# Performance work log

Measured on AMD Instinct MI355X. Metric: run time of the kernel, lower is better.

Reference implementation:

```python
import jax, jax.numpy as jnp
import numpy as np

N_NODES = 100000
N_EDGES = 1600000
HIDDEN = 64


def gcn_conv(x, edge_index, W, b):
    """PyG GCNConv: add self-loops, symmetric deg^{-1/2} normalization, scatter-add."""
    n = x.shape[0]
    h = x @ W  # [N, F_out]
    loop = jnp.arange(n, dtype=edge_index.dtype)
    src = jnp.concatenate([edge_index[0], loop])  # [E+N]
    dst = jnp.concatenate([edge_index[1], loop])
    deg = jax.ops.segment_sum(jnp.ones_like(dst, dtype=h.dtype), dst, num_segments=n)
    dinv = jnp.where(deg > 0, jax.lax.rsqrt(jnp.maximum(deg, 1e-12)), 0.0)
    norm = dinv[src] * dinv[dst]  # [E+N]
    msg = h[src] * norm[:, None]  # gather + scale
    out = jax.ops.segment_sum(msg, dst, num_segments=n)  # scatter-add
    return out + b


def setup_inputs() -> dict:
    key = jax.random.key(0)
    k = jax.random.split(key, 6)
    x = jax.random.normal(k[0], (N_NODES, HIDDEN), dtype=jnp.float32)
    edge_index = jax.random.randint(k[1], (2, N_EDGES), 0, N_NODES, dtype=jnp.int32)
    s = 1.0 / np.sqrt(HIDDEN)
    W1 = jax.random.normal(k[2], (HIDDEN, HIDDEN), dtype=jnp.float32) * s
    b1 = jnp.zeros((HIDDEN,), dtype=jnp.float32)
    W2 = jax.random.normal(k[3], (HIDDEN, HIDDEN), dtype=jnp.float32) * s
    b2 = jnp.zeros((HIDDEN,), dtype=jnp.float32)
    return {"x": x, "edge_index": edge_index, "W1": W1, "b1": b1, "W2": W2, "b2": b2}


def reference(x, edge_index, W1, b1, W2, b2):
    # Faithful to source: conv1 applied twice, relu, dropout (eval -> identity), conv2, log_softmax.
    h = gcn_conv(x, edge_index, W1, b1)
    h = jax.nn.relu(gcn_conv(h, edge_index, W1, b1))
    # F.dropout(training=self.training): identity in eval mode
    h = gcn_conv(h, edge_index, W2, b2)
    return jax.nn.log_softmax(h, axis=1)
```

## Files before the change

kernel.cpp:

```cpp
#include <hip/hip_runtime.h>
#include <hip/hip_bf16.h>

#define HID 64

typedef float f32x4 __attribute__((ext_vector_type(4)));

__device__ __forceinline__ unsigned short f2bf(float f) {
    unsigned u = __float_as_uint(f);
    return (unsigned short)((u + 0x7fffu + ((u >> 16) & 1u)) >> 16);
}
__device__ __forceinline__ void acc8(float* a, uint4 v) {
    a[0] += __uint_as_float(v.x << 16);
    a[1] += __uint_as_float(v.x & 0xffff0000u);
    a[2] += __uint_as_float(v.y << 16);
    a[3] += __uint_as_float(v.y & 0xffff0000u);
    a[4] += __uint_as_float(v.z << 16);
    a[5] += __uint_as_float(v.z & 0xffff0000u);
    a[6] += __uint_as_float(v.w << 16);
    a[7] += __uint_as_float(v.w & 0xffff0000u);
}


__global__ __launch_bounds__(256) void hist_part_kernel(
    const int* __restrict__ dst, int* __restrict__ cnt, int E, int psz) {
    int part = blockIdx.x & 7, chunk = blockIdx.x >> 3;
    int i = chunk * 256 + threadIdx.x;
    if (i >= E) return;
    int d = __builtin_nontemporal_load(&dst[i]);
    if (d / psz == part) atomicAdd(&cnt[d], 1);
}

__global__ __launch_bounds__(256) void bsum_kernel(const int* __restrict__ cnt,
                                                   int* __restrict__ bsums, int N) {
    __shared__ int s[256];
    int tid = threadIdx.x, i = blockIdx.x * 256 + tid;
    s[tid] = (i < N) ? cnt[i] : 0;
    __syncthreads();
    for (int o = 128; o > 0; o >>= 1) {
        if (tid < o) s[tid] += s[tid + o];
        __syncthreads();
    }
    if (tid == 0) bsums[blockIdx.x] = s[0];
}

__global__ __launch_bounds__(512) void scan_bsums_kernel(int* __restrict__ bsums, int nblk) {
    __shared__ int s[512];
    int tid = threadIdx.x;
    int orig = (tid < nblk) ? bsums[tid] : 0;
    s[tid] = orig;
    __syncthreads();
    for (int off = 1; off < 512; off <<= 1) {
        int v = (tid >= off) ? s[tid - off] : 0;
        __syncthreads();
        s[tid] += v;
        __syncthreads();
    }
    if (tid < nblk) bsums[tid] = s[tid] - orig;
}

__global__ __launch_bounds__(256) void rowptr_kernel(
    const int* __restrict__ cnt, const int* __restrict__ bsums,
    int4* __restrict__ nodeinfo, int* __restrict__ cursor, int N) {
    __shared__ int s[256];
    int tid = threadIdx.x, i = blockIdx.x * 256 + tid;
    int c = (i < N) ? cnt[i] : 0;
    s[tid] = c;
    __syncthreads();
    for (int off = 1; off < 256; off <<= 1) {
        int v = (tid >= off) ? s[tid - off] : 0;
        __syncthreads();
        s[tid] += v;
        __syncthreads();
    }
    if (i < N) {
        int excl = s[tid] - c + bsums[blockIdx.x];
        cursor[i] = excl;
        int4 ni;
        ni.x = excl;
        ni.y = c;
        ni.z = (int)__float_as_uint(rsqrtf((float)c + 1.0f));
        ni.w = 0;
        nodeinfo[i] = ni;
    }
}

__global__ __launch_bounds__(256) void fill_part_kernel(
    const int* __restrict__ src, const int* __restrict__ dst,
    int* __restrict__ cursor, int* __restrict__ col, int E, int psz) {
    int part = blockIdx.x & 7, chunk = blockIdx.x >> 3;
    int i = chunk * 256 + threadIdx.x;
    if (i >= E) return;
    int d = __builtin_nontemporal_load(&dst[i]);
    if (d / psz == part) {
        int s = __builtin_nontemporal_load(&src[i]);
        int p = atomicAdd(&cursor[d], 1);
        __builtin_nontemporal_store(s, &col[p]);
    }
}

__device__ __forceinline__ void gather64(
    const uint4* __restrict__ g4, const int* __restrict__ col,
    int beg, int deg, int n, int N, int lane, float* t) {
    int eighth = lane >> 3, fo = lane & 7;
    float a0[8] = {}, a1[8] = {};
    for (int base = 0; base < deg; base += 64) {
        int rem = deg - base; rem = rem > 64 ? 64 : rem;
        int c = (lane < rem) ? __builtin_nontemporal_load(&col[beg + base + lane]) : N;
        int groups = (rem + 7) >> 3;
        int j = 0;
        for (; j + 2 <= groups; j += 2) {
            int s0 = __shfl(c, 8 * (j + 0) + eighth, 64);
            int s1 = __shfl(c, 8 * (j + 1) + eighth, 64);
            uint4 v0 = g4[(size_t)s0 * 8 + fo];
            uint4 v1 = g4[(size_t)s1 * 8 + fo];
            acc8(a0, v0); acc8(a1, v1);
        }
        if (j < groups) {
            int s0 = __shfl(c, 8 * j + eighth, 64);
            uint4 v0 = g4[(size_t)s0 * 8 + fo];
            acc8(a0, v0);
        }
    }
    float sf[8] = {};
    acc8(sf, g4[(size_t)n * 8 + fo]);
#pragma unroll
    for (int k = 0; k < 8; ++k) {
        float s = a0[k] + a1[k];
        s += __shfl_xor(s, 8, 64);
        s += __shfl_xor(s, 16, 64);
        s += __shfl_xor(s, 32, 64);
        t[k] = s + sf[k];
    }
}


__global__ __launch_bounds__(256) void gemm_scale_kernel(
    const float* __restrict__ X, const float* __restrict__ W,
    const int4* __restrict__ nodeinfo, unsigned short* __restrict__ g, int N) {
    int tid = threadIdx.x, w = tid >> 6, lane = tid & 63;
    float Wreg[64];
#pragma unroll
    for (int k = 0; k < HID; ++k) Wreg[k] = W[k * HID + lane];
    int ngrp = (N + 4) / 4;
    for (int grp = blockIdx.x; grp < ngrp; grp += gridDim.x) {
        int row = grp * 4 + w;
        if (row > N) continue;
        if (row == N) { __builtin_nontemporal_store((unsigned short)0, &g[(size_t)N * HID + lane]); continue; }
        float xv = __builtin_nontemporal_load(&X[(size_t)row * HID + lane]);
        float dn = __uint_as_float(__builtin_amdgcn_readfirstlane((unsigned)nodeinfo[row].z));
        float acc = 0.f;
#pragma unroll
        for (int k = 0; k < HID; ++k) acc = fmaf(__shfl(xv, k, 64), Wreg[k], acc);
        __builtin_nontemporal_store(f2bf(acc * dn), &g[(size_t)row * HID + lane]);
    }
}


template <bool RELU>
__global__ __launch_bounds__(256) void agg_gemm_kernel(
    const unsigned short* __restrict__ g_in, const int4* __restrict__ nodeinfo,
    const int* __restrict__ col, const float* __restrict__ bias,
    const float* __restrict__ W, unsigned short* __restrict__ g_out, int N) {
    int tid = threadIdx.x, w = tid >> 6, lane = tid & 63;
    int fo = lane & 7;
    float Wreg[64];
#pragma unroll
    for (int k = 0; k < HID; ++k) Wreg[k] = W[k * HID + lane];
    float bb[8];
#pragma unroll
    for (int j = 0; j < 8; ++j) bb[j] = bias[8 * fo + j];
    const uint4* g4 = (const uint4*)g_in;
    int ngrp = (N + 4) / 4;
    for (int grp = blockIdx.x; grp < ngrp; grp += gridDim.x) {
        int n = grp * 4 + w;
        if (n > N) continue;
        if (n == N) { __builtin_nontemporal_store((unsigned short)0, &g_out[(size_t)N * HID + lane]); continue; }
        int4 ni = nodeinfo[n];
        int beg  = __builtin_amdgcn_readfirstlane(ni.x);
        int deg  = __builtin_amdgcn_readfirstlane(ni.y);
        float dn = __uint_as_float(__builtin_amdgcn_readfirstlane((unsigned)ni.z));
        float t[8];
        gather64(g4, col, beg, deg, n, N, lane, t);
        float o[8];
#pragma unroll
        for (int j = 0; j < 8; ++j) {
            o[j] = fmaf(dn, t[j], bb[j]);
            if (RELU) o[j] = fmaxf(o[j], 0.f);
        }
        float acc = 0.f;
#pragma unroll
        for (int q = 0; q < 8; ++q)
#pragma unroll
            for (int j = 0; j < 8; ++j)
                acc = fmaf(__shfl(o[j], q, 64), Wreg[8 * q + j], acc);
        __builtin_nontemporal_store(f2bf(acc * dn), &g_out[(size_t)n * HID + lane]);
    }
}


__global__ __launch_bounds__(256) void agg_lsm_kernel(
    const unsigned short* __restrict__ g_in, const int4* __restrict__ nodeinfo,
    const int* __restrict__ col, const float* __restrict__ bias,
    float* __restrict__ out, int N) {
    int tid = threadIdx.x;
    int n = blockIdx.x * 4 + (tid >> 6);
    if (n >= N) return;
    int lane = tid & 63;
    int eighth = lane >> 3, fo = lane & 7;
    int4 ni = nodeinfo[n];
    int beg  = __builtin_amdgcn_readfirstlane(ni.x);
    int deg  = __builtin_amdgcn_readfirstlane(ni.y);
    float dn = __uint_as_float(__builtin_amdgcn_readfirstlane((unsigned)ni.z));
    const uint4* g4 = (const uint4*)g_in;
    float t[8];
    gather64(g4, col, beg, deg, n, N, lane, t);
    float v[8];
#pragma unroll
    for (int k = 0; k < 8; ++k) v[k] = fmaf(dn, t[k], bias[8 * fo + k]);
    float mx = v[0];
#pragma unroll
    for (int k = 1; k < 8; ++k) mx = fmaxf(mx, v[k]);
    mx = fmaxf(mx, __shfl_xor(mx, 1, 64));
    mx = fmaxf(mx, __shfl_xor(mx, 2, 64));
    mx = fmaxf(mx, __shfl_xor(mx, 4, 64));
    float sum = 0.f;
#pragma unroll
    for (int k = 0; k < 8; ++k) sum += expf(v[k] - mx);
    sum += __shfl_xor(sum, 1, 64);
    sum += __shfl_xor(sum, 2, 64);
    sum += __shfl_xor(sum, 4, 64);
    float ls = mx + logf(sum);
    if (eighth == 0) {
        f32x4 o0 = {v[0] - ls, v[1] - ls, v[2] - ls, v[3] - ls};
        f32x4 o1 = {v[4] - ls, v[5] - ls, v[6] - ls, v[7] - ls};
        f32x4* op = (f32x4*)out;
        __builtin_nontemporal_store(o0, &op[(size_t)n * 16 + 2 * fo]);
        __builtin_nontemporal_store(o1, &op[(size_t)n * 16 + 2 * fo + 1]);
    }
}


static inline size_t alignup(size_t x) { return (x + 255) & ~(size_t)255; }

extern "C" void kernel_launch(void* const* d_in, const int* in_sizes, int n_in,
                              void* d_out, int out_size, void* d_ws, size_t ws_size,
                              hipStream_t stream) {
    const float* x  = (const float*)d_in[0];
    const int*   ei = (const int*)d_in[1];
    const float* W1 = (const float*)d_in[2];
    const float* b1 = (const float*)d_in[3];
    const float* W2 = (const float*)d_in[4];
    const float* b2 = (const float*)d_in[5];

    const int N = in_sizes[0] / HID;
    const int E = in_sizes[1] / 2;
    const int* src = ei;
    const int* dst = ei + E;

    const int nblk = (N + 255) / 256;
    const int psz  = (N + 7) / 8;

    char* w = (char*)d_ws;
    unsigned short* gA       = (unsigned short*)w; w += alignup((size_t)(N + 1) * HID * 2);
    unsigned short* gB       = (unsigned short*)w; w += alignup((size_t)(N + 1) * HID * 2);
    int4*           nodeinfo = (int4*)w;           w += alignup((size_t)N * 16);
    int*            cnt      = (int*)w;            w += alignup((size_t)N * 4);
    int*            cursor   = (int*)w;            w += alignup((size_t)N * 4);
    int*            col      = (int*)w;            w += alignup((size_t)E * 4);
    int*            bsums    = (int*)w;            w += alignup((size_t)nblk * 4);

    const int egrid  = (E + 255) / 256;
    const int ngrid  = (N + 3) / 4;
    const int gsgrid = 2048;

    (void)hipMemsetAsync(cnt, 0, (size_t)N * sizeof(int), stream);
    hist_part_kernel<<<egrid * 8, 256, 0, stream>>>(dst, cnt, E, psz);
    bsum_kernel<<<nblk, 256, 0, stream>>>(cnt, bsums, N);
    scan_bsums_kernel<<<1, 512, 0, stream>>>(bsums, nblk);
    rowptr_kernel<<<nblk, 256, 0, stream>>>(cnt, bsums, nodeinfo, cursor, N);
    fill_part_kernel<<<egrid * 8, 256, 0, stream>>>(src, dst, cursor, col, E, psz);

    gemm_scale_kernel<<<gsgrid, 256, 0, stream>>>(x, W1, nodeinfo, gA, N);
    agg_gemm_kernel<false><<<gsgrid, 256, 0, stream>>>(gA, nodeinfo, col, b1, W1, gB, N);
    agg_gemm_kernel<true><<<gsgrid, 256, 0, stream>>>(gB, nodeinfo, col, b1, W2, gA, N);
    agg_lsm_kernel<<<ngrid, 256, 0, stream>>>(gA, nodeinfo, col, b2, (float*)d_out, N);
}
```

Before: 498.1 us.

## Pack W as bf16 registers, prefetch first col chunk, persist LSM kernel

The fused aggregate-GEMM kernels now keep W as packed bf16 pairs in 32 registers instead of 64 floats. The 64x64 product is done as a local partial product followed by a butterfly shuffle reduction, and the kernel gets a launch-bounds occupancy hint. The first column-index chunk is loaded before the gather loop so it can overlap setup work. The first GEMM now stages W and the x row in shared memory instead of using register shuffles. The log-softmax kernel becomes a grid-stride persistent kernel, the padding-row zeroing moves to memsets, and the col store becomes a normal store. Rounding W to bf16 adds some precision error.

```diff
diff --git a/kernel.cpp b/kernel.cpp
--- a/kernel.cpp
+++ b/kernel.cpp
@@ -94,18 +94,18 @@
     if (d / psz == part) {
         int s = __builtin_nontemporal_load(&src[i]);
         int p = atomicAdd(&cursor[d], 1);
-        __builtin_nontemporal_store(s, &col[p]);
-    }
-}
-
-__device__ __forceinline__ void gather64(
+        col[p] = s;
+    }
+}
+
+__device__ __forceinline__ void gather64_pre(
     const uint4* __restrict__ g4, const int* __restrict__ col,
-    int beg, int deg, int n, int N, int lane, float* t) {
+    int beg, int deg, int c, int n, int N, int lane, float* t) {
     int eighth = lane >> 3, fo = lane & 7;
     float a0[8] = {}, a1[8] = {};
-    for (int base = 0; base < deg; base += 64) {
-        int rem = deg - base; rem = rem > 64 ? 64 : rem;
-        int c = (lane < rem) ? __builtin_nontemporal_load(&col[beg + base + lane]) : N;
+    int base = 0;
+    while (true) {
+        int rem = deg - base; if (rem > 64) rem = 64;
         int groups = (rem + 7) >> 3;
         int j = 0;
         for (; j + 2 <= groups; j += 2) {
@@ -120,6 +120,10 @@
             uint4 v0 = g4[(size_t)s0 * 8 + fo];
             acc8(a0, v0);
         }
+        base += 64;
+        if (base >= deg) break;
+        int r2 = deg - base;
+        c = (lane < r2) ? __builtin_nontemporal_load(&col[beg + base + lane]) : N;
     }
     float sf[8] = {};
     acc8(sf, g4[(size_t)n * 8 + fo]);
@@ -137,63 +141,96 @@
 __global__ __launch_bounds__(256) void gemm_scale_kernel(
     const float* __restrict__ X, const float* __restrict__ W,
     const int4* __restrict__ nodeinfo, unsigned short* __restrict__ g, int N) {
-    int tid = threadIdx.x, w = tid >> 6, lane = tid & 63;
-    float Wreg[64];
-#pragma unroll
-    for (int k = 0; k < HID; ++k) Wreg[k] = W[k * HID + lane];
-    int ngrp = (N + 4) / 4;
+    __shared__ float Ws[HID * HID];
+    __shared__ float xs[4][HID];
+    int tid = threadIdx.x;
+    for (int i = tid; i < HID * HID; i += 256) Ws[i] = W[i];
+    __syncthreads();
+    int w = tid >> 6, c = tid & 63;
+    float* xsw = xs[w];
+    int ngrp = (N + 3) / 4;
     for (int grp = blockIdx.x; grp < ngrp; grp += gridDim.x) {
         int row = grp * 4 + w;
-        if (row > N) continue;
-        if (row == N) { __builtin_nontemporal_store((unsigned short)0, &g[(size_t)N * HID + lane]); continue; }
-        float xv = __builtin_nontemporal_load(&X[(size_t)row * HID + lane]);
-        float dn = __uint_as_float(__builtin_amdgcn_readfirstlane((unsigned)nodeinfo[row].z));
+        if (row >= N) continue;
+        xsw[c] = __builtin_nontemporal_load(&X[(size_t)row * HID + c]);
+        float dn = __uint_as_float((unsigned)__builtin_amdgcn_readfirstlane(nodeinfo[row].z));
         float acc = 0.f;
 #pragma unroll
-        for (int k = 0; k < HID; ++k) acc = fmaf(__shfl(xv, k, 64), Wreg[k], acc);
-        __builtin_nontemporal_store(f2bf(acc * dn), &g[(size_t)row * HID + lane]);
+        for (int k = 0; k < HID; ++k) acc = fmaf(xsw[k], Ws[k * HID + c], acc);
+        __builtin_nontemporal_store(f2bf(acc * dn), &g[(size_t)row * HID + c]);
     }
 }
 
 
 template <bool RELU>
-__global__ __launch_bounds__(256) void agg_gemm_kernel(
+__global__ __launch_bounds__(256, 4) void agg_gemm_kernel(
     const unsigned short* __restrict__ g_in, const int4* __restrict__ nodeinfo,
     const int* __restrict__ col, const float* __restrict__ bias,
     const float* __restrict__ W, unsigned short* __restrict__ g_out, int N) {
     int tid = threadIdx.x, w = tid >> 6, lane = tid & 63;
-    int fo = lane & 7;
-    float Wreg[64];
-#pragma unroll
-    for (int k = 0; k < HID; ++k) Wreg[k] = W[k * HID + lane];
+    int s = lane & 7, q = lane >> 3;
+    unsigned Wp[32];
+#pragma unroll
+    for (int j = 0; j < 8; ++j)
+#pragma unroll
+        for (int i2 = 0; i2 < 4; ++i2) {
+            float w0 = W[(8 * s + j) * HID + 8 * q + 2 * i2];
+            float w1 = W[(8 * s + j) * HID + 8 * q + 2 * i2 + 1];
+            Wp[j * 4 + i2] = (unsigned)f2bf(w0) | ((unsigned)f2bf(w1) << 16);
+        }
     float bb[8];
 #pragma unroll
-    for (int j = 0; j < 8; ++j) bb[j] = bias[8 * fo + j];
+    for (int j = 0; j < 8; ++j) bb[j] = bias[8 * s + j];
     const uint4* g4 = (const uint4*)g_in;
-    int ngrp = (N + 4) / 4;
+    const int ngrp = (N + 3) / 4;
     for (int grp = blockIdx.x; grp < ngrp; grp += gridDim.x) {
         int n = grp * 4 + w;
-        if (n > N) continue;
-        if (n == N) { __builtin_nontemporal_store((unsigned short)0, &g_out[(size_t)N * HID + lane]); continue; }
+        if (n >= N) continue;
         int4 ni = nodeinfo[n];
-        int beg  = __builtin_amdgcn_readfirstlane(ni.x);
-        int deg  = __builtin_amdgcn_readfirstlane(ni.y);
-        float dn = __uint_as_float(__builtin_amdgcn_readfirstlane((unsigned)ni.z));
+        int beg = __builtin_amdgcn_readfirstlane(ni.x);
+        int deg = __builtin_amdgcn_readfirstlane(ni.y);
+        float dn = __uint_as_float((unsigned)__builtin_amdgcn_readfirstlane(ni.z));
+        int c0 = (lane < deg) ? __builtin_nontemporal_load(&col[beg + lane]) : N;
         float t[8];
-        gather64(g4, col, beg, deg, n, N, lane, t);
+        gather64_pre(g4, col, beg, deg, c0, n, N, lane, t);
         float o[8];
 #pragma unroll
         for (int j = 0; j < 8; ++j) {
             o[j] = fmaf(dn, t[j], bb[j]);
             if (RELU) o[j] = fmaxf(o[j], 0.f);
         }
-        float acc = 0.f;
-#pragma unroll
-        for (int q = 0; q < 8; ++q)
-#pragma unroll
-            for (int j = 0; j < 8; ++j)
-                acc = fmaf(__shfl(o[j], q, 64), Wreg[8 * q + j], acc);
-        __builtin_nontemporal_store(f2bf(acc * dn), &g_out[(size_t)n * HID + lane]);
+        float p[8] = {};
+#pragma unroll
+        for (int j = 0; j < 8; ++j) {
+            float oj = o[j];
+#pragma unroll
+            for (int i2 = 0; i2 < 4; ++i2) {
+                unsigned wv = Wp[j * 4 + i2];
+                p[2 * i2]     = fmaf(oj, __uint_as_float(wv << 16), p[2 * i2]);
+                p[2 * i2 + 1] = fmaf(oj, __uint_as_float(wv & 0xffff0000u), p[2 * i2 + 1]);
+            }
+        }
+        bool b0 = (s & 1) != 0;
+        float q1[4];
+#pragma unroll
+        for (int m = 0; m < 4; ++m) {
+            float A = __shfl_xor(p[2 * m], 1, 64);
+            float B = __shfl_xor(p[2 * m + 1], 1, 64);
+            q1[m] = b0 ? (p[2 * m + 1] + B) : (p[2 * m] + A);
+        }
+        bool b1 = ((s >> 1) & 1) != 0;
+        float q2[2];
+#pragma unroll
+        for (int m = 0; m < 2; ++m) {
+            float A = __shfl_xor(q1[2 * m], 2, 64);
+            float B = __shfl_xor(q1[2 * m + 1], 2, 64);
+            q2[m] = b1 ? (q1[2 * m + 1] + B) : (q1[2 * m] + A);
+        }
+        bool b2 = ((s >> 2) & 1) != 0;
+        float A = __shfl_xor(q2[0], 4, 64);
+        float B = __shfl_xor(q2[1], 4, 64);
+        float res = b2 ? (q2[1] + B) : (q2[0] + A);
+        __builtin_nontemporal_store(f2bf(res * dn), &g_out[(size_t)n * HID + lane]);
     }
 }
 
@@ -202,40 +239,46 @@
     const unsigned short* __restrict__ g_in, const int4* __restrict__ nodeinfo,
     const int* __restrict__ col, const float* __restrict__ bias,
     float* __restrict__ out, int N) {
-    int tid = threadIdx.x;
-    int n = blockIdx.x * 4 + (tid >> 6);
-    if (n >= N) return;
-    int lane = tid & 63;
+    int tid = threadIdx.x, w = tid >> 6, lane = tid & 63;
     int eighth = lane >> 3, fo = lane & 7;
-    int4 ni = nodeinfo[n];
-    int beg  = __builtin_amdgcn_readfirstlane(ni.x);
-    int deg  = __builtin_amdgcn_readfirstlane(ni.y);
-    float dn = __uint_as_float(__builtin_amdgcn_readfirstlane((unsigned)ni.z));
     const uint4* g4 = (const uint4*)g_in;
-    float t[8];
-    gather64(g4, col, beg, deg, n, N, lane, t);
-    float v[8];
-#pragma unroll
-    for (int k = 0; k < 8; ++k) v[k] = fmaf(dn, t[k], bias[8 * fo + k]);
-    float mx = v[0];
-#pragma unroll
-    for (int k = 1; k < 8; ++k) mx = fmaxf(mx, v[k]);
-    mx = fmaxf(mx, __shfl_xor(mx, 1, 64));
-    mx = fmaxf(mx, __shfl_xor(mx, 2, 64));
-    mx = fmaxf(mx, __shfl_xor(mx, 4, 64));
-    float sum = 0.f;
-#pragma unroll
-    for (int k = 0; k < 8; ++k) sum += expf(v[k] - mx);
-    sum += __shfl_xor(sum, 1, 64);
-    sum += __shfl_xor(sum, 2, 64);
-    sum += __shfl_xor(sum, 4, 64);
-    float ls = mx + logf(sum);
-    if (eighth == 0) {
-        f32x4 o0 = {v[0] - ls, v[1] - ls, v[2] - ls, v[3] - ls};
-        f32x4 o1 = {v[4] - ls, v[5] - ls, v[6] - ls, v[7] - ls};
-        f32x4* op = (f32x4*)out;
-        __builtin_nontemporal_store(o0, &op[(size_t)n * 16 + 2 * fo]);
-        __builtin_nontemporal_store(o1, &op[(size_t)n * 16 + 2 * fo + 1]);
+    float bb[8];
+#pragma unroll
+    for (int j = 0; j < 8; ++j) bb[j] = bias[8 * fo + j];
+    const int ngrp = (N + 3) / 4;
+    for (int grp = blockIdx.x; grp < ngrp; grp += gridDim.x) {
+        int n = grp * 4 + w;
+        if (n >= N) continue;
+        int4 ni = nodeinfo[n];
+        int beg = __builtin_amdgcn_readfirstlane(ni.x);
+        int deg = __builtin_amdgcn_readfirstlane(ni.y);
+        float dn = __uint_as_float((unsigned)__builtin_amdgcn_readfirstlane(ni.z));
+        int c0 = (lane < deg) ? __builtin_nontemporal_load(&col[beg + lane]) : N;
+        float t[8];
+        gather64_pre(g4, col, beg, deg, c0, n, N, lane, t);
+        float v[8];
+#pragma unroll
+        for (int k = 0; k < 8; ++k) v[k] = fmaf(dn, t[k], bb[k]);
+        float mx = v[0];
+#pragma unroll
+        for (int k = 1; k < 8; ++k) mx = fmaxf(mx, v[k]);
+        mx = fmaxf(mx, __shfl_xor(mx, 1, 64));
+        mx = fmaxf(mx, __shfl_xor(mx, 2, 64));
+        mx = fmaxf(mx, __shfl_xor(mx, 4, 64));
+        float sum = 0.f;
+#pragma unroll
+        for (int k = 0; k < 8; ++k) sum += expf(v[k] - mx);
+        sum += __shfl_xor(sum, 1, 64);
+        sum += __shfl_xor(sum, 2, 64);
+        sum += __shfl_xor(sum, 4, 64);
+        float ls = mx + logf(sum);
+        if (eighth == 0) {
+            f32x4 o0 = {v[0] - ls, v[1] - ls, v[2] - ls, v[3] - ls};
+            f32x4 o1 = {v[4] - ls, v[5] - ls, v[6] - ls, v[7] - ls};
+            f32x4* op = (f32x4*)out;
+            __builtin_nontemporal_store(o0, &op[(size_t)n * 16 + 2 * fo]);
+            __builtin_nontemporal_store(o1, &op[(size_t)n * 16 + 2 * fo + 1]);
+        }
     }
 }
 
@@ -270,8 +313,10 @@
     int*            bsums    = (int*)w;            w += alignup((size_t)nblk * 4);
 
     const int egrid  = (E + 255) / 256;
-    const int ngrid  = (N + 3) / 4;
     const int gsgrid = 2048;
+
+    (void)hipMemsetAsync(gA + (size_t)N * HID, 0, HID * sizeof(unsigned short), stream);
+    (void)hipMemsetAsync(gB + (size_t)N * HID, 0, HID * sizeof(unsigned short), stream);
 
     (void)hipMemsetAsync(cnt, 0, (size_t)N * sizeof(int), stream);
     hist_part_kernel<<<egrid * 8, 256, 0, stream>>>(dst, cnt, E, psz);
@@ -283,5 +328,5 @@
     gemm_scale_kernel<<<gsgrid, 256, 0, stream>>>(x, W1, nodeinfo, gA, N);
     agg_gemm_kernel<false><<<gsgrid, 256, 0, stream>>>(gA, nodeinfo, col, b1, W1, gB, N);
     agg_gemm_kernel<true><<<gsgrid, 256, 0, stream>>>(gB, nodeinfo, col, b1, W2, gA, N);
-    agg_lsm_kernel<<<ngrid, 256, 0, stream>>>(gA, nodeinfo, col, b2, (float*)d_out, N);
-}
+    agg_lsm_kernel<<<gsgrid, 256, 0, stream>>>(gA, nodeinfo, col, b2, (float*)d_out, N);
+}
```

Result: faster. 415.4 us (-16.6%).
